# Kernel tuning notes

Measured on AMD Instinct MI355X. Metric: run time of the kernel, lower is better.

Reference implementation:

```python
import jax, jax.numpy as jnp
import numpy as np

B, S, D = 2, 2048, 1024
H, DK, DV = 16, 64, 64
D_OUT = 1024


def setup_inputs() -> dict:
    key = jax.random.key(0)
    ks = jax.random.split(key, 9)
    sd = 1.0 / np.sqrt(D)
    # Linear weights stored as [in, out] (torch applies x @ W.T with W [out,in])
    return {
        "x": jax.random.normal(ks[0], (B, S, D), dtype=jnp.float32),
        "Wq": jax.random.normal(ks[1], (D, H * DK), dtype=jnp.float32) * sd,
        "bq": jnp.zeros((H * DK,), dtype=jnp.float32),
        "Wk": jax.random.normal(ks[2], (D, H * DK), dtype=jnp.float32) * sd,
        "bk": jnp.zeros((H * DK,), dtype=jnp.float32),
        "Wv": jax.random.normal(ks[3], (D, H * DV), dtype=jnp.float32) * sd,
        "bv": jnp.zeros((H * DV,), dtype=jnp.float32),
        "Wo": jax.random.normal(ks[4], (H * DV, D_OUT), dtype=jnp.float32) * sd,
        "bo": jnp.zeros((D_OUT,), dtype=jnp.float32),
    }


def _attn(x, Wq, bq, Wk, bk, Wv, bv, Wo, bo):
    n = x.shape[-2]
    q = (x @ Wq + bq).reshape(B, n, H, DK).transpose(0, 2, 1, 3)  # [B,H,S,DK]
    k = (x @ Wk + bk).reshape(B, n, H, DK).transpose(0, 2, 1, 3)
    v = (x @ Wv + bv).reshape(B, n, H, DV).transpose(0, 2, 1, 3)
    scores = jnp.einsum("bhqd,bhkd->bhqk", q / jnp.sqrt(jnp.float32(DK)), k)
    # causal additive mask: 0 on/below diagonal, -inf above (matches 1 - 1/tril)
    causal = jnp.tril(jnp.ones((n, n), dtype=bool))
    scores = jnp.where(causal, scores, -jnp.inf)
    probs = jax.nn.softmax(scores, axis=-1)
    out = jnp.einsum("bhqk,bhkd->bhqd", probs, v)  # [B,H,S,DV]
    out = out.transpose(0, 2, 1, 3).reshape(B, n, H * DV)
    return out @ Wo + bo


def reference(x, Wq, bq, Wk, bk, Wv, bv, Wo, bo):
    return _attn(x, Wq, bq, Wk, bk, Wv, bv, Wo, bo)
```

## Files before the change

### kernel.cpp

```cpp
#include <hip/hip_runtime.h>

typedef unsigned short u16;
typedef __bf16 bf16_t;
typedef bf16_t bf16x8 __attribute__((ext_vector_type(8)));
typedef float f32x4 __attribute__((ext_vector_type(4)));

#define DEV __device__ __forceinline__
#define LOG2E 1.4426950408889634f
#define QKS (0.125f * LOG2E)

static_assert(sizeof(bf16x8) == 16, "bf16x8 must be 16B");

DEV u16 f2b(float v) { return __builtin_bit_cast(u16, (bf16_t)v); }
DEV float b2f(u16 v) { return (float)__builtin_bit_cast(bf16_t, v); }

DEV void g2l16(const void* g, void* l) {
  __builtin_amdgcn_global_load_lds(
      (const __attribute__((address_space(1))) void*)g,
      (__attribute__((address_space(3))) void*)l, 16, 0, 0);
}

DEV int sniff_is_f32(const u16* __restrict__ W) {
  const int lane = threadIdx.x & 63;
  int cnt = 0;
#pragma unroll
  for (int i = 0; i < 8; i++) {
    u16 u = W[(lane * 8 + i) * 2];
    cnt += (((u >> 7) & 0xFF) >= 126) ? 1 : 0;
  }
#pragma unroll
  for (int off = 1; off < 64; off <<= 1) cnt += __shfl_xor(cnt, off, 64);
  return cnt > 128;
}


__global__ __launch_bounds__(256) void convert_x_k(
    const void* __restrict__ xin, const u16* __restrict__ Wsniff,
    u16* __restrict__ xb) {
  const int i = (blockIdx.x * 256 + threadIdx.x) * 8;
  if (sniff_is_f32(Wsniff)) {
    const float* xf = (const float*)xin;
    float4 a = *(const float4*)&xf[i];
    float4 b = *(const float4*)&xf[i + 4];
    u16 o[8] = {f2b(a.x), f2b(a.y), f2b(a.z), f2b(a.w),
                f2b(b.x), f2b(b.y), f2b(b.z), f2b(b.w)};
    *(uint4*)&xb[i] = *(const uint4*)o;
  } else {
    *(uint4*)&xb[i] = *(const uint4*)((const u16*)xin + i);
  }
}

__global__ __launch_bounds__(256) void transpose_k(
    const void* __restrict__ Wq, const void* __restrict__ Wk,
    const void* __restrict__ Wv, const void* __restrict__ Wo,
    const void* __restrict__ bq, const void* __restrict__ bk,
    const void* __restrict__ bv, const void* __restrict__ bo,
    u16* __restrict__ Wqkv_t, u16* __restrict__ Wo_t,
    u16* __restrict__ bqkv_b, u16* __restrict__ bo_b) {
  __shared__ u16 tile[64][68];
  const int z = blockIdx.z;
  const void* src = (z == 0) ? Wq : (z == 1) ? Wk : (z == 2) ? Wv : Wo;
  u16* dst = (z < 3) ? (Wqkv_t + (size_t)z * 1024 * 1024) : Wo_t;
  const int k0 = blockIdx.y * 64, n0 = blockIdx.x * 64;
  const int t = threadIdx.x;
  const int r = t >> 4, c4 = (t & 15) * 4;
  const int isf = sniff_is_f32((const u16*)Wq);

  if (blockIdx.x == 0 && blockIdx.y == 0) {
    const void* bsrc = (z == 0) ? bq : (z == 1) ? bk : (z == 2) ? bv : bo;
    u16* bdst = (z < 3) ? (bqkv_b + z * 1024) : bo_b;
#pragma unroll
    for (int i = 0; i < 4; i++) {
      const int idx = t + i * 256;
      const float v =
          isf ? ((const float*)bsrc)[idx] : b2f(((const u16*)bsrc)[idx]);
      bdst[idx] = f2b(v);
    }
  }

#pragma unroll
  for (int i = 0; i < 4; i++) {
    int rr = r + i * 16;
    const size_t base = (size_t)(k0 + rr) * 1024 + n0 + c4;
    if (isf) {
      float4 v = *(const float4*)((const float*)src + base);
      tile[rr][c4] = f2b(v.x); tile[rr][c4 + 1] = f2b(v.y);
      tile[rr][c4 + 2] = f2b(v.z); tile[rr][c4 + 3] = f2b(v.w);
    } else {
      ushort4 v = *(const ushort4*)((const u16*)src + base);
      tile[rr][c4] = v.x; tile[rr][c4 + 1] = v.y;
      tile[rr][c4 + 2] = v.z; tile[rr][c4 + 3] = v.w;
    }
  }
  __syncthreads();
#pragma unroll
  for (int i = 0; i < 4; i++) {
    int rr = r + i * 16;
    ushort4 v;
    v.x = tile[c4][rr]; v.y = tile[c4 + 1][rr];
    v.z = tile[c4 + 2][rr]; v.w = tile[c4 + 3][rr];
    *(ushort4*)&dst[(size_t)(n0 + rr) * 1024 + k0 + c4] = v;
  }
}

template <int MODE>
__global__ __launch_bounds__(256, 3) void gemm_k(
    const u16* __restrict__ A, const u16* __restrict__ Bt,
    const u16* __restrict__ bias, void* __restrict__ o0v,
    u16* __restrict__ o1, u16* __restrict__ o2,
    const u16* __restrict__ Wsniff, int M, int N, int K) {
  alignas(16) __shared__ u16 As[128][32];
  alignas(16) __shared__ u16 Bs[128][32];
  const int tid = threadIdx.x;
  const int wave = tid >> 6, lane = tid & 63;
  const int quad = lane >> 4, l16 = lane & 15;
  const int m0 = blockIdx.y * 128, n0 = blockIdx.x * 128;
  const int wr = (wave >> 1) * 64, wc = (wave & 1) * 64;

  f32x4 acc[4][4];
#pragma unroll
  for (int i = 0; i < 4; i++)
#pragma unroll
    for (int j = 0; j < 4; j++) acc[i][j] = (f32x4){0.f, 0.f, 0.f, 0.f};

  const int srow = lane >> 2, scol = (lane & 3) * 8;
  for (int k0 = 0; k0 < K; k0 += 32) {
    __syncthreads();
#pragma unroll
    for (int j = 0; j < 4; j++) {
      const int t = wave * 4 + j;
      if (t < 8) {
        const int row = t * 16 + srow;
        g2l16(&A[(size_t)(m0 + row) * K + k0 + scol], &As[t * 16][0]);
      } else {
        const int rb = t - 8;
        const int row = rb * 16 + srow;
        g2l16(&Bt[(size_t)(n0 + row) * K + k0 + scol], &Bs[rb * 16][0]);
      }
    }
    __syncthreads();
    bf16x8 af[4], bfr[4];
#pragma unroll
    for (int mi = 0; mi < 4; mi++)
      af[mi] = *(const bf16x8*)&As[wr + mi * 16 + l16][quad * 8];
#pragma unroll
    for (int ni = 0; ni < 4; ni++)
      bfr[ni] = *(const bf16x8*)&Bs[wc + ni * 16 + l16][quad * 8];
#pragma unroll
    for (int mi = 0; mi < 4; mi++)
#pragma unroll
      for (int ni = 0; ni < 4; ni++)
        acc[mi][ni] = __builtin_amdgcn_mfma_f32_16x16x32_bf16(
            af[mi], bfr[ni], acc[mi][ni], 0, 0, 0);
  }

  const int isf = (MODE == 1) ? sniff_is_f32(Wsniff) : 0;
#pragma unroll
  for (int mi = 0; mi < 4; mi++) {
    const int rbase = m0 + wr + mi * 16 + quad * 4;
#pragma unroll
    for (int ni = 0; ni < 4; ni++) {
      const int col = n0 + wc + ni * 16 + l16;
      const float bv_ = b2f(bias[col]);
      if (MODE == 0) {
        const int seg = col >> 10;
        const int nn = col & 1023;
        const int h = nn >> 6, d = nn & 63;
        u16* op = (seg == 0) ? (u16*)o0v : (seg == 1) ? o1 : o2;
#pragma unroll
        for (int r = 0; r < 4; r++) {
          const int m = rbase + r;
          const int b = m >> 11, s = m & 2047;
          float v = acc[mi][ni][r] + bv_;
          if (seg == 0) v *= QKS;
          if (seg < 2)
            op[(((size_t)(b * 16 + h) * 2048) + s) * 64 + d] = f2b(v);
          else
            op[(((size_t)(b * 16 + h) * 64) + d) * 2048 + s] = f2b(v);
        }
      } else {
#pragma unroll
        for (int r = 0; r < 4; r++) {
          const int m = rbase + r;
          const float v = acc[mi][ni][r] + bv_;
          if (isf) ((float*)o0v)[(size_t)m * N + col] = v;
          else     ((u16*)o0v)[(size_t)m * N + col] = f2b(v);
        }
      }
    }
  }
}

__global__ __launch_bounds__(256, 1) void attn_k(
    const u16* __restrict__ Q, const u16* __restrict__ K,
    const u16* __restrict__ Vt, u16* __restrict__ O) {
  alignas(16) __shared__ u16 Ks[2][128][64];
  alignas(16) __shared__ u16 Vs[2][64][128];
  alignas(16) __shared__ u16 Ps[128][72];
  const int tid = threadIdx.x;
  const int wave = tid >> 6, lane = tid & 63;
  const int quad = lane >> 4, l16 = lane & 15;
  const int bh = blockIdx.y;
  const int b = bh >> 4, h = bh & 15;
  const int sw = l16 & 7;

  const int krow_off = lane >> 3, kchunk = lane & 7;
  const int vrow_off = lane >> 4, vchunk = lane & 15;

  for (int pi = 0; pi < 2; pi++) {
    const int qt = pi ? (15 - (int)blockIdx.x) : (int)blockIdx.x;
    const int q0 = qt * 128;
    const int wrow = q0 + wave * 32;
    const int nkt = qt + 1;

    bf16x8 aq[2][2];
#pragma unroll
    for (int mi = 0; mi < 2; mi++)
#pragma unroll
      for (int kcD = 0; kcD < 2; kcD++)
        aq[mi][kcD] = *(const bf16x8*)&Q[((size_t)bh * 2048 + wrow + mi * 16 +
                                          l16) * 64 + kcD * 32 + quad * 8];

    f32x4 oacc[2][4];
#pragma unroll
    for (int mi = 0; mi < 2; mi++)
#pragma unroll
      for (int di = 0; di < 4; di++) oacc[mi][di] = (f32x4){0.f, 0.f, 0.f, 0.f};
    float lrow[2][4] = {{0.f, 0.f, 0.f, 0.f}, {0.f, 0.f, 0.f, 0.f}};

    auto stage = [&](int buf, int kts) {
      const int k0s = kts * 128;
#pragma unroll
      for (int j = 0; j < 8; j++) {
        const int t = wave * 8 + j;
        if (t < 16) {
          const int r = t * 8 + krow_off;
          const int cs = kchunk ^ (r & 7);
          g2l16(&K[((size_t)bh * 2048 + k0s + r) * 64 + cs * 8],
                &Ks[buf][t * 8][0]);
        } else {
          const int t2 = t - 16;
          const int r = t2 * 4 + vrow_off;
          const int cs = vchunk ^ (r & 7);
          g2l16(&Vt[((size_t)bh * 64 + r) * 2048 + k0s + cs * 8],
                &Vs[buf][t2 * 4][0]);
        }
      }
    };

    stage(0, 0);
    for (int kt = 0; kt < nkt; kt++) {
      const int cur = kt & 1;
      const int k0 = kt * 128;
      if (kt + 1 < nkt) {
        stage(cur ^ 1, kt + 1);
        asm volatile("s_waitcnt vmcnt(8)" ::: "memory");
      } else {
        asm volatile("s_waitcnt vmcnt(0)" ::: "memory");
      }
      asm volatile("s_barrier" ::: "memory");

      for (int h2 = 0; h2 < 2; h2++) {
        const int k0h = k0 + h2 * 64;
        if (k0h > wrow + 31) continue;
        const bool needmask = (k0h + 63 > wrow);

        f32x4 sacc[2][4];
#pragma unroll
        for (int mi = 0; mi < 2; mi++)
#pragma unroll
          for (int ni = 0; ni < 4; ni++)
            sacc[mi][ni] = (f32x4){0.f, 0.f, 0.f, 0.f};
#pragma unroll
        for (int kcD = 0; kcD < 2; kcD++)
#pragma unroll
          for (int ni = 0; ni < 4; ni++) {
            const int pos = ((kcD << 2) | quad) ^ sw;
            bf16x8 bk_ =
                *(const bf16x8*)&Ks[cur][h2 * 64 + ni * 16 + l16][pos * 8];
#pragma unroll
            for (int mi = 0; mi < 2; mi++)
              sacc[mi][ni] = __builtin_amdgcn_mfma_f32_16x16x32_bf16(
                  aq[mi][kcD], bk_, sacc[mi][ni], 0, 0, 0);
          }

#pragma unroll
        for (int mi = 0; mi < 2; mi++) {
          const int rowb = wrow + mi * 16 + quad * 4;
#pragma unroll
          for (int ni = 0; ni < 4; ni++) {
            const int col = k0h + ni * 16 + l16;
#pragma unroll
            for (int r = 0; r < 4; r++) {
              float p = __builtin_amdgcn_exp2f(sacc[mi][ni][r]);
              if (needmask && (col > rowb + r)) p = 0.f;
              lrow[mi][r] += p;
              Ps[wave * 32 + mi * 16 + quad * 4 + r][ni * 16 + l16] = f2b(p);
            }
          }
        }
        asm volatile("s_waitcnt lgkmcnt(0)" ::: "memory");

#pragma unroll
        for (int kc = 0; kc < 2; kc++) {
          bf16x8 ap[2];
#pragma unroll
          for (int mi = 0; mi < 2; mi++)
            ap[mi] = *(const bf16x8*)&Ps[wave * 32 + mi * 16 + l16]
                                        [kc * 32 + quad * 8];
#pragma unroll
          for (int di = 0; di < 4; di++) {
            const int pos = ((h2 << 3) | (kc << 2) | quad) ^ sw;
            bf16x8 bv_ = *(const bf16x8*)&Vs[cur][di * 16 + l16][pos * 8];
#pragma unroll
            for (int mi = 0; mi < 2; mi++)
              oacc[mi][di] = __builtin_amdgcn_mfma_f32_16x16x32_bf16(
                  ap[mi], bv_, oacc[mi][di], 0, 0, 0);
          }
        }
      }
      asm volatile("s_barrier" ::: "memory");
    }

#pragma unroll
    for (int mi = 0; mi < 2; mi++)
#pragma unroll
      for (int r = 0; r < 4; r++) {
#pragma unroll
        for (int off = 1; off < 16; off <<= 1)
          lrow[mi][r] += __shfl_xor(lrow[mi][r], off, 64);
      }

#pragma unroll
    for (int mi = 0; mi < 2; mi++)
#pragma unroll
      for (int di = 0; di < 4; di++)
#pragma unroll
        for (int r = 0; r < 4; r++) {
          const int row = wrow + mi * 16 + quad * 4 + r;
          const float v = oacc[mi][di][r] / lrow[mi][r];
          O[((size_t)b * 2048 + row) * 1024 + h * 64 + di * 16 + l16] = f2b(v);
        }
  }
}

extern "C" void kernel_launch(void* const* d_in, const int* in_sizes, int n_in,
                              void* d_out, int out_size, void* d_ws,
                              size_t ws_size, hipStream_t stream) {
  const void* x  = d_in[0];
  const void* Wq = d_in[1];
  const void* bq = d_in[2];
  const void* Wk = d_in[3];
  const void* bk = d_in[4];
  const void* Wv = d_in[5];
  const void* bv = d_in[6];
  const void* Wo = d_in[7];
  const void* bo = d_in[8];

  char* ws = (char*)d_ws;
  u16* xb     = (u16*)ws;          ws += (size_t)4096 * 1024 * 2;
  u16* Wqkv_t = (u16*)ws;          ws += (size_t)3072 * 1024 * 2;
  u16* Wo_t   = (u16*)ws;          ws += (size_t)1024 * 1024 * 2;
  u16* bqkv_b = (u16*)ws;          ws += 3072 * 2;
  u16* bo_b   = (u16*)ws;          ws += 1024 * 2 + 128;
  u16* Qb     = (u16*)ws;          ws += (size_t)4096 * 1024 * 2;
  u16* Kb     = (u16*)ws;          ws += (size_t)4096 * 1024 * 2;
  u16* Vtb    = (u16*)ws;          ws += (size_t)4096 * 1024 * 2;
  u16* Ob     = xb;

  convert_x_k<<<2048, 256, 0, stream>>>(x, (const u16*)Wq, xb);
  transpose_k<<<dim3(16, 16, 4), 256, 0, stream>>>(Wq, Wk, Wv, Wo, bq, bk, bv,
                                                   bo, Wqkv_t, Wo_t, bqkv_b,
                                                   bo_b);
  gemm_k<0><<<dim3(24, 32), 256, 0, stream>>>(xb, Wqkv_t, bqkv_b, Qb, Kb, Vtb,
                                              (const u16*)Wq, 4096, 3072, 1024);
  attn_k<<<dim3(8, 32), 256, 0, stream>>>(Qb, Kb, Vtb, Ob);
  gemm_k<1><<<dim3(8, 32), 256, 0, stream>>>(Ob, Wo_t, bo_b, d_out, nullptr,
                                             nullptr, (const u16*)Wq, 4096,
                                             1024, 1024);
}
```

Before: 225.7 us.

## Use 8 waves per attention block with transposed S computation and swizzled P tile

```diff
diff --git a/kernel.cpp b/kernel.cpp
--- a/kernel.cpp
+++ b/kernel.cpp
@@ -191,14 +191,14 @@
   }
 }
 
-__global__ __launch_bounds__(256, 1) void attn_k(
+__global__ __launch_bounds__(512, 4) void attn_k(
     const u16* __restrict__ Q, const u16* __restrict__ K,
     const u16* __restrict__ Vt, u16* __restrict__ O) {
   alignas(16) __shared__ u16 Ks[2][128][64];
   alignas(16) __shared__ u16 Vs[2][64][128];
-  alignas(16) __shared__ u16 Ps[128][72];
+  alignas(16) __shared__ u16 PsT[128][64];
   const int tid = threadIdx.x;
-  const int wave = tid >> 6, lane = tid & 63;
+  const int w = tid >> 6, lane = tid & 63;
   const int quad = lane >> 4, l16 = lane & 15;
   const int bh = blockIdx.y;
   const int b = bh >> 4, h = bh & 15;
@@ -210,29 +210,25 @@
   for (int pi = 0; pi < 2; pi++) {
     const int qt = pi ? (15 - (int)blockIdx.x) : (int)blockIdx.x;
     const int q0 = qt * 128;
-    const int wrow = q0 + wave * 32;
+    const int wrow = q0 + w * 16;
     const int nkt = qt + 1;
 
-    bf16x8 aq[2][2];
-#pragma unroll
-    for (int mi = 0; mi < 2; mi++)
-#pragma unroll
-      for (int kcD = 0; kcD < 2; kcD++)
-        aq[mi][kcD] = *(const bf16x8*)&Q[((size_t)bh * 2048 + wrow + mi * 16 +
-                                          l16) * 64 + kcD * 32 + quad * 8];
-
-    f32x4 oacc[2][4];
-#pragma unroll
-    for (int mi = 0; mi < 2; mi++)
-#pragma unroll
-      for (int di = 0; di < 4; di++) oacc[mi][di] = (f32x4){0.f, 0.f, 0.f, 0.f};
-    float lrow[2][4] = {{0.f, 0.f, 0.f, 0.f}, {0.f, 0.f, 0.f, 0.f}};
+    bf16x8 aq[2];
+#pragma unroll
+    for (int kc = 0; kc < 2; kc++)
+      aq[kc] = *(const bf16x8*)&Q[((size_t)bh * 2048 + wrow + l16) * 64 +
+                                  kc * 32 + quad * 8];
+
+    f32x4 oacc[4];
+#pragma unroll
+    for (int di = 0; di < 4; di++) oacc[di] = (f32x4){0.f, 0.f, 0.f, 0.f};
+    float lrp = 0.f;
 
     auto stage = [&](int buf, int kts) {
       const int k0s = kts * 128;
 #pragma unroll
-      for (int j = 0; j < 8; j++) {
-        const int t = wave * 8 + j;
+      for (int j = 0; j < 4; j++) {
+        const int t = w * 4 + j;
         if (t < 16) {
           const int r = t * 8 + krow_off;
           const int cs = kchunk ^ (r & 7);
@@ -254,93 +250,81 @@
       const int k0 = kt * 128;
       if (kt + 1 < nkt) {
         stage(cur ^ 1, kt + 1);
-        asm volatile("s_waitcnt vmcnt(8)" ::: "memory");
+        asm volatile("s_waitcnt vmcnt(4)" ::: "memory");
       } else {
         asm volatile("s_waitcnt vmcnt(0)" ::: "memory");
       }
       asm volatile("s_barrier" ::: "memory");
 
+#pragma unroll
       for (int h2 = 0; h2 < 2; h2++) {
         const int k0h = k0 + h2 * 64;
-        if (k0h > wrow + 31) continue;
+        if (k0h > wrow + 15) continue;
         const bool needmask = (k0h + 63 > wrow);
 
-        f32x4 sacc[2][4];
-#pragma unroll
-        for (int mi = 0; mi < 2; mi++)
-#pragma unroll
-          for (int ni = 0; ni < 4; ni++)
-            sacc[mi][ni] = (f32x4){0.f, 0.f, 0.f, 0.f};
-#pragma unroll
-        for (int kcD = 0; kcD < 2; kcD++)
-#pragma unroll
-          for (int ni = 0; ni < 4; ni++) {
-            const int pos = ((kcD << 2) | quad) ^ sw;
-            bf16x8 bk_ =
-                *(const bf16x8*)&Ks[cur][h2 * 64 + ni * 16 + l16][pos * 8];
-#pragma unroll
-            for (int mi = 0; mi < 2; mi++)
-              sacc[mi][ni] = __builtin_amdgcn_mfma_f32_16x16x32_bf16(
-                  aq[mi][kcD], bk_, sacc[mi][ni], 0, 0, 0);
+        f32x4 st[4];
+#pragma unroll
+        for (int nk = 0; nk < 4; nk++) st[nk] = (f32x4){0.f, 0.f, 0.f, 0.f};
+#pragma unroll
+        for (int kc = 0; kc < 2; kc++)
+#pragma unroll
+          for (int nk = 0; nk < 4; nk++) {
+            const int pos = ((kc << 2) | quad) ^ sw;
+            bf16x8 kf =
+                *(const bf16x8*)&Ks[cur][h2 * 64 + nk * 16 + l16][pos * 8];
+            st[nk] = __builtin_amdgcn_mfma_f32_16x16x32_bf16(kf, aq[kc],
+                                                             st[nk], 0, 0, 0);
           }
 
-#pragma unroll
-        for (int mi = 0; mi < 2; mi++) {
-          const int rowb = wrow + mi * 16 + quad * 4;
-#pragma unroll
-          for (int ni = 0; ni < 4; ni++) {
-            const int col = k0h + ni * 16 + l16;
-#pragma unroll
-            for (int r = 0; r < 4; r++) {
-              float p = __builtin_amdgcn_exp2f(sacc[mi][ni][r]);
-              if (needmask && (col > rowb + r)) p = 0.f;
-              lrow[mi][r] += p;
-              Ps[wave * 32 + mi * 16 + quad * 4 + r][ni * 16 + l16] = f2b(p);
-            }
+        const int q_glob = wrow + l16;
+#pragma unroll
+        for (int nk = 0; nk < 4; nk++) {
+          const int kbase = k0h + nk * 16 + quad * 4;
+          u16 pk[4];
+#pragma unroll
+          for (int r = 0; r < 4; r++) {
+            float p = __builtin_amdgcn_exp2f(st[nk][r]);
+            if (needmask && (kbase + r > q_glob)) p = 0.f;
+            lrp += p;
+            pk[r] = f2b(p);
           }
+          const int g = nk * 4 + quad;
+          const int cc = (g >> 1) ^ sw;
+          *(uint2*)&PsT[w * 16 + l16][cc * 8 + (g & 1) * 4] =
+              *(const uint2*)pk;
         }
         asm volatile("s_waitcnt lgkmcnt(0)" ::: "memory");
 
 #pragma unroll
         for (int kc = 0; kc < 2; kc++) {
-          bf16x8 ap[2];
-#pragma unroll
-          for (int mi = 0; mi < 2; mi++)
-            ap[mi] = *(const bf16x8*)&Ps[wave * 32 + mi * 16 + l16]
-                                        [kc * 32 + quad * 8];
+          const int pcc = ((kc << 2) | quad) ^ sw;
+          bf16x8 ap = *(const bf16x8*)&PsT[w * 16 + l16][pcc * 8];
 #pragma unroll
           for (int di = 0; di < 4; di++) {
             const int pos = ((h2 << 3) | (kc << 2) | quad) ^ sw;
-            bf16x8 bv_ = *(const bf16x8*)&Vs[cur][di * 16 + l16][pos * 8];
-#pragma unroll
-            for (int mi = 0; mi < 2; mi++)
-              oacc[mi][di] = __builtin_amdgcn_mfma_f32_16x16x32_bf16(
-                  ap[mi], bv_, oacc[mi][di], 0, 0, 0);
+            bf16x8 vf = *(const bf16x8*)&Vs[cur][di * 16 + l16][pos * 8];
+            oacc[di] = __builtin_amdgcn_mfma_f32_16x16x32_bf16(ap, vf,
+                                                               oacc[di], 0, 0, 0);
           }
         }
       }
       asm volatile("s_barrier" ::: "memory");
     }
 
-#pragma unroll
-    for (int mi = 0; mi < 2; mi++)
+    lrp += __shfl_xor(lrp, 16, 64);
+    lrp += __shfl_xor(lrp, 32, 64);
+    float rdiv[4];
+#pragma unroll
+    for (int r = 0; r < 4; r++) rdiv[r] = __shfl(lrp, quad * 4 + r, 64);
+
+#pragma unroll
+    for (int di = 0; di < 4; di++)
 #pragma unroll
       for (int r = 0; r < 4; r++) {
-#pragma unroll
-        for (int off = 1; off < 16; off <<= 1)
-          lrow[mi][r] += __shfl_xor(lrow[mi][r], off, 64);
-      }
-
-#pragma unroll
-    for (int mi = 0; mi < 2; mi++)
-#pragma unroll
-      for (int di = 0; di < 4; di++)
-#pragma unroll
-        for (int r = 0; r < 4; r++) {
-          const int row = wrow + mi * 16 + quad * 4 + r;
-          const float v = oacc[mi][di][r] / lrow[mi][r];
-          O[((size_t)b * 2048 + row) * 1024 + h * 64 + di * 16 + l16] = f2b(v);
-        }
+        const int row = wrow + quad * 4 + r;
+        const float v = oacc[di][r] / rdiv[r];
+        O[((size_t)b * 2048 + row) * 1024 + h * 64 + di * 16 + l16] = f2b(v);
+      }
   }
 }
 
@@ -374,7 +358,7 @@
                                                    bo_b);
   gemm_k<0><<<dim3(24, 32), 256, 0, stream>>>(xb, Wqkv_t, bqkv_b, Qb, Kb, Vtb,
                                               (const u16*)Wq, 4096, 3072, 1024);
-  attn_k<<<dim3(8, 32), 256, 0, stream>>>(Qb, Kb, Vtb, Ob);
+  attn_k<<<dim3(8, 32), 512, 0, stream>>>(Qb, Kb, Vtb, Ob);
   gemm_k<1><<<dim3(8, 32), 256, 0, stream>>>(Ob, Wo_t, bo_b, d_out, nullptr,
                                              nullptr, (const u16*)Wq, 4096,
                                              1024, 1024);
```

Measured after the change: 210.6 us. 6.7% less time.
